# Performance work log

Measured on AMD Instinct MI355X. Metric: run time of the kernel, lower is better.

The kernel has to match this reference:

```python
import jax, jax.numpy as jnp
import numpy as np

B, T, D, HS = 8, 2048, 1024, 64  # batch, seq, num_embd, head_size


def setup_inputs() -> dict:
    key = jax.random.key(0)
    kc, kq, kk, kv = jax.random.split(key, 4)
    return {
        "context": jax.random.normal(kc, (B, T, D), dtype=jnp.float32),
        "Wq": jax.random.normal(kq, (D, HS), dtype=jnp.float32) * (D ** -0.5),
        "Wk": jax.random.normal(kk, (D, HS), dtype=jnp.float32) * (D ** -0.5),
        "Wv": jax.random.normal(kv, (D, HS), dtype=jnp.float32) * (D ** -0.5),
    }


def reference(context, Wq, Wk, Wv):
    # context: [B, T, D]; projections: [B, T, HS]
    q = context @ Wq
    k = context @ Wk
    v = context @ Wv
    scale = k.shape[-1] ** -0.5
    # scores: [B, T, T], causal mask, stable softmax (dropout p=0 -> identity)
    wei = jnp.einsum("btd,bsd->bts", q, k) * scale
    t = wei.shape[-1]
    causal = jnp.tril(jnp.ones((t, t), dtype=bool))
    wei = jnp.where(causal, wei, -jnp.inf)
    wei = jax.nn.softmax(wei, axis=-1)
    return jnp.einsum("bts,bsh->bth", wei, v)
```

## Files before the change

### kernel.cpp

```cpp
#include <hip/hip_runtime.h>
#include <math.h>

#define BB 8
#define TT 2048
#define DD 1024
#define HSZ 64

typedef __bf16 bf16_t;
typedef bf16_t bf16x8 __attribute__((ext_vector_type(8)));
typedef bf16_t bf16x4 __attribute__((ext_vector_type(4)));
typedef float f32x4 __attribute__((ext_vector_type(4)));

#define MFMA16(A, B, C) __builtin_amdgcn_mfma_f32_16x16x32_bf16(A, B, C, 0, 0, 0)


__global__ __launch_bounds__(256) void wt_convert(
    const float* __restrict__ Wq, const float* __restrict__ Wk,
    const float* __restrict__ Wv, bf16_t* __restrict__ Wtf)
{
    int id = blockIdx.x * 256 + threadIdx.x;
    int j = id & 7;
    int lane = (id >> 3) & 63;
    int chunk = (id >> 9) & 31;
    int nt = id >> 14;
    int l16 = lane & 15, quad = lane >> 4;
    int k = chunk * 32 + quad * 8 + j;
    int col = nt * 16 + l16;
    int m = col >> 6, ncol = col & 63;
    const float* W = (m == 0) ? Wq : (m == 1) ? Wk : Wv;
    float scl = (m == 0) ? 0.18033688f : 1.0f;
    Wtf[id] = (bf16_t)(W[k * HSZ + ncol] * scl);
}

__global__ __launch_bounds__(256, 2) void qkv_proj(
    const float* __restrict__ ctx, const bf16_t* __restrict__ Wtf,
    bf16_t* __restrict__ Q, bf16_t* __restrict__ Kf, bf16_t* __restrict__ Vf)
{
    __shared__ f32x4 red[4][12][64];

    const int tid = threadIdx.x;
    const int w = tid >> 6, lane = tid & 63;
    const int quad = lane >> 4, l16 = lane & 15;
    const size_t row0 = (size_t)blockIdx.x * 16;
    const int k0 = w * 256;

    f32x4 acc[12];
    #pragma unroll
    for (int i = 0; i < 12; ++i) acc[i] = (f32x4){0.f, 0.f, 0.f, 0.f};

    const float* arow = ctx + (row0 + l16) * DD + k0 + quad * 8;
    const bf16_t* wbase = Wtf + lane * 8;

    bf16x8 bfr[2][12];
    {
        const int chunk0 = k0 >> 5;
        #pragma unroll
        for (int nt = 0; nt < 12; ++nt)
            bfr[0][nt] = *(const bf16x8*)(wbase + ((size_t)nt * 32 + chunk0) * 512);
    }
    float4 a0 = *(const float4*)(arow);
    float4 a1 = *(const float4*)(arow + 4);

    #pragma unroll
    for (int kc = 0; kc < 256; kc += 32) {
        const int cur = (kc >> 5) & 1;
        bf16x8 af;
        af[0] = (bf16_t)a0.x; af[1] = (bf16_t)a0.y;
        af[2] = (bf16_t)a0.z; af[3] = (bf16_t)a0.w;
        af[4] = (bf16_t)a1.x; af[5] = (bf16_t)a1.y;
        af[6] = (bf16_t)a1.z; af[7] = (bf16_t)a1.w;

        if (kc + 32 < 256) {
            const int chunk = (k0 + kc + 32) >> 5;
            #pragma unroll
            for (int nt = 0; nt < 12; ++nt)
                bfr[cur ^ 1][nt] =
                    *(const bf16x8*)(wbase + ((size_t)nt * 32 + chunk) * 512);
            a0 = *(const float4*)(arow + kc + 32);
            a1 = *(const float4*)(arow + kc + 36);
        }

        #pragma unroll
        for (int nt = 0; nt < 12; ++nt)
            acc[nt] = MFMA16(af, bfr[cur][nt], acc[nt]);
    }

    #pragma unroll
    for (int nt = 0; nt < 12; ++nt) red[w][nt][lane] = acc[nt];
    __syncthreads();

    const int bb   = (int)(row0 >> 11);
    const int tloc = (int)(row0 & 2047);
    const int kt   = tloc >> 6;
    const int nn   = (tloc >> 4) & 3;

    #pragma unroll
    for (int i = 0; i < 3; ++i) {
        const int nt = w * 3 + i;
        f32x4 s = red[0][nt][lane];
        s += red[1][nt][lane];
        s += red[2][nt][lane];
        s += red[3][nt][lane];

        const int m = nt >> 2;
        if (m == 0) {
            const int col = (nt & 3) * 16 + l16;
            #pragma unroll
            for (int reg = 0; reg < 4; ++reg)
                Q[(row0 + quad * 4 + reg) * HSZ + col] = (bf16_t)s[reg];
        } else if (m == 1) {
            const int g = nt - 4;
            const int ks = g >> 1;
            const int quadf = (g & 1) * 2 + (l16 >> 3);
            const int jj = l16 & 7;
            const size_t fb = ((((size_t)bb * 32 + kt) * 4 + nn) * 2 + ks) * 512;
            #pragma unroll
            for (int reg = 0; reg < 4; ++reg)
                Kf[fb + (quadf * 16 + quad * 4 + reg) * 8 + jj] = (bf16_t)s[reg];
        } else {
            const int dt = nt - 8;
            const int t0 = tloc + quad * 4;
            const int ks = (t0 >> 5) & 1;
            const int quadf = (t0 >> 3) & 3;
            const int j0 = t0 & 7;
            const size_t fb = ((((size_t)bb * 32 + kt) * 2 + ks) * 4 + dt) * 512;
            bf16x4 v;
            #pragma unroll
            for (int reg = 0; reg < 4; ++reg) v[reg] = (bf16_t)s[reg];
            *(bf16x4*)(Vf + fb + (quadf * 16 + l16) * 8 + j0) = v;
        }
    }
}

__device__ __forceinline__ void load_kfrags(
    const bf16_t* __restrict__ Kf, size_t bofs, int kt, int lane, int nv,
    bf16x8* kf)
{
    const bf16_t* kbase = Kf + ((bofs + (size_t)kt) * 8) * 512 + lane * 8;
    #pragma unroll
    for (int n = 0; n < 4; ++n) {
        if (n < nv) {
            kf[2 * n]     = *(const bf16x8*)(kbase + (n * 2) * 512);
            kf[2 * n + 1] = *(const bf16x8*)(kbase + (n * 2 + 1) * 512);
        }
    }
}

__global__ __launch_bounds__(64, 3) void attn_kernel(
    const bf16_t* __restrict__ Q, const bf16_t* __restrict__ Kf,
    const bf16_t* __restrict__ Vf,
    float* __restrict__ Opart, float* __restrict__ Lpart)
{
    __shared__ bf16_t Ps[16][76];

    const int lane = threadIdx.x;
    const int quad = lane >> 4, l16 = lane & 15;

    const int z = blockIdx.x;
    const int b = z & 7, c = z >> 3;
    const int j = 127 - (c >> 2);
    const int seg = c & 3;
    const size_t base = (size_t)b * TT * HSZ;
    const size_t bofs = (size_t)b * 32;
    const int ntile = (j >> 2) + 1, jm = j & 3;

    const bf16_t* qp = Q + base + (size_t)(j * 16 + l16) * HSZ + quad * 8;
    bf16x8 qf0 = *(const bf16x8*)qp;
    bf16x8 qf1 = *(const bf16x8*)(qp + 32);

    bf16x8 onesf;
    {
        bf16_t e = (l16 == 0) ? (bf16_t)1.0f : (bf16_t)0.0f;
        #pragma unroll
        for (int i = 0; i < 8; ++i) onesf[i] = e;
    }

    f32x4 o[4];
    #pragma unroll
    for (int dt = 0; dt < 4; ++dt) o[dt] = (f32x4){0.f, 0.f, 0.f, 0.f};
    f32x4 lacc = (f32x4){0.f, 0.f, 0.f, 0.f};

    bf16x8 kA[8], kB[8];

    auto process = [&](int kt, const bf16x8* kf) {
        const bool last = (kt == ntile - 1);
        const int nv = last ? jm + 1 : 4;
        const int ksm = (nv > 2) ? 2 : 1;

        const bf16_t* vbase = Vf + ((bofs + (size_t)kt) * 8) * 512 + lane * 8;
        bf16x8 vf[8];
        #pragma unroll
        for (int dt = 0; dt < 4; ++dt) {
            vf[2 * dt] = *(const bf16x8*)(vbase + dt * 512);
            if (ksm == 2) vf[2 * dt + 1] = *(const bf16x8*)(vbase + (4 + dt) * 512);
        }

        f32x4 sc[4];
        #pragma unroll
        for (int n = 0; n < 4; ++n) {
            if (n < nv) {
                f32x4 a = (f32x4){0.f, 0.f, 0.f, 0.f};
                a = MFMA16(qf0, kf[2 * n], a);
                a = MFMA16(qf1, kf[2 * n + 1], a);
                sc[n] = a;
            }
        }

        if (last) {
            #pragma unroll
            for (int n = 0; n < 4; ++n) {
                if (n < nv) {
                    #pragma unroll
                    for (int reg = 0; reg < 4; ++reg) {
                        bool masked = (n == jm) && (l16 > quad * 4 + reg);
                        float p = __builtin_amdgcn_exp2f(sc[n][reg]);
                        sc[n][reg] = masked ? 0.f : p;
                    }
                }
            }
        } else {
            #pragma unroll
            for (int n = 0; n < 4; ++n)
                #pragma unroll
                for (int reg = 0; reg < 4; ++reg)
                    sc[n][reg] = __builtin_amdgcn_exp2f(sc[n][reg]);
        }

        #pragma unroll
        for (int n = 0; n < 4; ++n) {
            #pragma unroll
            for (int reg = 0; reg < 4; ++reg) {
                float p = (n < nv) ? sc[n][reg] : 0.f;
                Ps[quad * 4 + reg][n * 16 + l16] = (bf16_t)p;
            }
        }
        bf16x8 pf0 = *(const bf16x8*)&Ps[l16][quad * 8];
        bf16x8 pf1 = *(const bf16x8*)&Ps[l16][32 + quad * 8];

        #pragma unroll
        for (int dt = 0; dt < 4; ++dt) {
            o[dt] = MFMA16(pf0, vf[2 * dt], o[dt]);
            if (ksm == 2) o[dt] = MFMA16(pf1, vf[2 * dt + 1], o[dt]);
        }
        lacc = MFMA16(pf0, onesf, lacc);
        if (ksm == 2) lacc = MFMA16(pf1, onesf, lacc);
    };

    auto nv_of = [&](int kt) { return (kt == ntile - 1) ? jm + 1 : 4; };

    if (seg < ntile) {
        load_kfrags(Kf, bofs, seg, lane, nv_of(seg), kA);
        for (int kt = seg; kt < ntile; kt += 8) {
            if (kt + 4 < ntile) load_kfrags(Kf, bofs, kt + 4, lane, nv_of(kt + 4), kB);
            process(kt, kA);
            if (kt + 4 < ntile) {
                if (kt + 8 < ntile) load_kfrags(Kf, bofs, kt + 8, lane, nv_of(kt + 8), kA);
                process(kt + 4, kB);
            }
        }
    }

    float* op = Opart + (size_t)z * 16 * 64;
    #pragma unroll
    for (int dt = 0; dt < 4; ++dt) {
        #pragma unroll
        for (int reg = 0; reg < 4; ++reg)
            op[(quad * 4 + reg) * 64 + dt * 16 + l16] = o[dt][reg];
    }
    if (l16 == 0) {
        #pragma unroll
        for (int reg = 0; reg < 4; ++reg)
            Lpart[z * 16 + quad * 4 + reg] = lacc[reg];
    }
}

__global__ __launch_bounds__(256) void combine_kernel(
    const float* __restrict__ Opart, const float* __restrict__ Lpart,
    float* __restrict__ O)
{
    int gid = blockIdx.x * 256 + threadIdx.x;
    int col = gid & 63;
    int row = (gid >> 6) & 15;
    int j   = (gid >> 10) & 127;
    int b   = gid >> 17;
    int z0 = ((127 - j) * 4) * 8 + b;
    float l = 0.f, ov = 0.f;
    #pragma unroll
    for (int s = 0; s < 4; ++s) {
        l  += Lpart[(z0 + 8 * s) * 16 + row];
        ov += Opart[((size_t)(z0 + 8 * s) * 16 + row) * 64 + col];
    }
    O[((size_t)b * TT + j * 16 + row) * 64 + col] = ov / l;
}

extern "C" void kernel_launch(void* const* d_in, const int* in_sizes, int n_in,
                              void* d_out, int out_size, void* d_ws, size_t ws_size,
                              hipStream_t stream) {
    const float* ctx = (const float*)d_in[0];
    const float* Wq  = (const float*)d_in[1];
    const float* Wk  = (const float*)d_in[2];
    const float* Wv  = (const float*)d_in[3];
    float* out = (float*)d_out;

    const size_t NQ = (size_t)BB * TT * HSZ;
    bf16_t* Qw  = (bf16_t*)d_ws;
    bf16_t* Kfw = Qw + NQ;
    bf16_t* Vfw = Kfw + NQ;
    bf16_t* Wtf = Vfw + NQ;
    float*  Opart = (float*)(Wtf + 196608);
    float*  Lpart = Opart + (size_t)4096 * 1024;

    wt_convert<<<768, 256, 0, stream>>>(Wq, Wk, Wv, Wtf);
    qkv_proj<<<1024, 256, 0, stream>>>(ctx, Wtf, Qw, Kfw, Vfw);
    attn_kernel<<<4096, 64, 0, stream>>>(Qw, Kfw, Vfw, Opart, Lpart);
    combine_kernel<<<4096, 256, 0, stream>>>(Opart, Lpart, out);
}
```

Before: 140.4 us.

## Cut projection register/LDS footprint and make attention K/V loads unconditional

The QKV projection drops its double-buffered weight fragments and does its cross-wave reduction in three rounds through a smaller shared buffer. This allows three blocks per CU instead of two, at the cost of software prefetch and extra barriers. The attention kernel now always loads all eight K and V fragments, removing per-fragment branches. This may load data that is never used on the last causal tile, in exchange for simpler, more uniform load code.

```diff
diff --git a/kernel.cpp b/kernel.cpp
--- a/kernel.cpp
+++ b/kernel.cpp
@@ -32,11 +32,11 @@
     Wtf[id] = (bf16_t)(W[k * HSZ + ncol] * scl);
 }
 
-__global__ __launch_bounds__(256, 2) void qkv_proj(
+__global__ __launch_bounds__(256, 3) void qkv_proj(
     const float* __restrict__ ctx, const bf16_t* __restrict__ Wtf,
     bf16_t* __restrict__ Q, bf16_t* __restrict__ Kf, bf16_t* __restrict__ Vf)
 {
-    __shared__ f32x4 red[4][12][64];
+    __shared__ f32x4 red[4][4][64];
 
     const int tid = threadIdx.x;
     const int w = tid >> 6, lane = tid & 63;
@@ -51,43 +51,24 @@
     const float* arow = ctx + (row0 + l16) * DD + k0 + quad * 8;
     const bf16_t* wbase = Wtf + lane * 8;
 
-    bf16x8 bfr[2][12];
-    {
-        const int chunk0 = k0 >> 5;
+    #pragma unroll
+    for (int kc = 0; kc < 256; kc += 32) {
+        const int chunk = (k0 + kc) >> 5;
+        bf16x8 bfr[12];
         #pragma unroll
         for (int nt = 0; nt < 12; ++nt)
-            bfr[0][nt] = *(const bf16x8*)(wbase + ((size_t)nt * 32 + chunk0) * 512);
-    }
-    float4 a0 = *(const float4*)(arow);
-    float4 a1 = *(const float4*)(arow + 4);
-
-    #pragma unroll
-    for (int kc = 0; kc < 256; kc += 32) {
-        const int cur = (kc >> 5) & 1;
+            bfr[nt] = *(const bf16x8*)(wbase + ((size_t)nt * 32 + chunk) * 512);
+        float4 a0 = *(const float4*)(arow + kc);
+        float4 a1 = *(const float4*)(arow + kc + 4);
         bf16x8 af;
         af[0] = (bf16_t)a0.x; af[1] = (bf16_t)a0.y;
         af[2] = (bf16_t)a0.z; af[3] = (bf16_t)a0.w;
         af[4] = (bf16_t)a1.x; af[5] = (bf16_t)a1.y;
         af[6] = (bf16_t)a1.z; af[7] = (bf16_t)a1.w;
-
-        if (kc + 32 < 256) {
-            const int chunk = (k0 + kc + 32) >> 5;
-            #pragma unroll
-            for (int nt = 0; nt < 12; ++nt)
-                bfr[cur ^ 1][nt] =
-                    *(const bf16x8*)(wbase + ((size_t)nt * 32 + chunk) * 512);
-            a0 = *(const float4*)(arow + kc + 32);
-            a1 = *(const float4*)(arow + kc + 36);
-        }
-
         #pragma unroll
         for (int nt = 0; nt < 12; ++nt)
-            acc[nt] = MFMA16(af, bfr[cur][nt], acc[nt]);
-    }
-
-    #pragma unroll
-    for (int nt = 0; nt < 12; ++nt) red[w][nt][lane] = acc[nt];
-    __syncthreads();
+            acc[nt] = MFMA16(af, bfr[nt], acc[nt]);
+    }
 
     const int bb   = (int)(row0 >> 11);
     const int tloc = (int)(row0 & 2047);
@@ -95,35 +76,36 @@
     const int nn   = (tloc >> 4) & 3;
 
     #pragma unroll
-    for (int i = 0; i < 3; ++i) {
-        const int nt = w * 3 + i;
-        f32x4 s = red[0][nt][lane];
-        s += red[1][nt][lane];
-        s += red[2][nt][lane];
-        s += red[3][nt][lane];
-
-        const int m = nt >> 2;
-        if (m == 0) {
-            const int col = (nt & 3) * 16 + l16;
+    for (int r = 0; r < 3; ++r) {
+        if (r) __syncthreads();
+        #pragma unroll
+        for (int i = 0; i < 4; ++i) red[w][i][lane] = acc[r * 4 + i];
+        __syncthreads();
+
+        f32x4 s = red[0][w][lane];
+        s += red[1][w][lane];
+        s += red[2][w][lane];
+        s += red[3][w][lane];
+
+        if (r == 0) {
+            const int col = w * 16 + l16;
             #pragma unroll
             for (int reg = 0; reg < 4; ++reg)
                 Q[(row0 + quad * 4 + reg) * HSZ + col] = (bf16_t)s[reg];
-        } else if (m == 1) {
-            const int g = nt - 4;
-            const int ks = g >> 1;
-            const int quadf = (g & 1) * 2 + (l16 >> 3);
+        } else if (r == 1) {
+            const int ks = w >> 1;
+            const int quadf = (w & 1) * 2 + (l16 >> 3);
             const int jj = l16 & 7;
             const size_t fb = ((((size_t)bb * 32 + kt) * 4 + nn) * 2 + ks) * 512;
             #pragma unroll
             for (int reg = 0; reg < 4; ++reg)
                 Kf[fb + (quadf * 16 + quad * 4 + reg) * 8 + jj] = (bf16_t)s[reg];
         } else {
-            const int dt = nt - 8;
             const int t0 = tloc + quad * 4;
             const int ks = (t0 >> 5) & 1;
             const int quadf = (t0 >> 3) & 3;
             const int j0 = t0 & 7;
-            const size_t fb = ((((size_t)bb * 32 + kt) * 2 + ks) * 4 + dt) * 512;
+            const size_t fb = ((((size_t)bb * 32 + kt) * 2 + ks) * 4 + w) * 512;
             bf16x4 v;
             #pragma unroll
             for (int reg = 0; reg < 4; ++reg) v[reg] = (bf16_t)s[reg];
@@ -133,17 +115,12 @@
 }
 
 __device__ __forceinline__ void load_kfrags(
-    const bf16_t* __restrict__ Kf, size_t bofs, int kt, int lane, int nv,
-    bf16x8* kf)
+    const bf16_t* __restrict__ Kf, size_t bofs, int kt, int lane, bf16x8* kf)
 {
     const bf16_t* kbase = Kf + ((bofs + (size_t)kt) * 8) * 512 + lane * 8;
     #pragma unroll
-    for (int n = 0; n < 4; ++n) {
-        if (n < nv) {
-            kf[2 * n]     = *(const bf16x8*)(kbase + (n * 2) * 512);
-            kf[2 * n + 1] = *(const bf16x8*)(kbase + (n * 2 + 1) * 512);
-        }
-    }
+    for (int i = 0; i < 8; ++i)
+        kf[i] = *(const bf16x8*)(kbase + i * 512);
 }
 
 __global__ __launch_bounds__(64, 3) void attn_kernel(
@@ -190,10 +167,8 @@
         const bf16_t* vbase = Vf + ((bofs + (size_t)kt) * 8) * 512 + lane * 8;
         bf16x8 vf[8];
         #pragma unroll
-        for (int dt = 0; dt < 4; ++dt) {
-            vf[2 * dt] = *(const bf16x8*)(vbase + dt * 512);
-            if (ksm == 2) vf[2 * dt + 1] = *(const bf16x8*)(vbase + (4 + dt) * 512);
-        }
+        for (int i = 0; i < 8; ++i)
+            vf[i] = *(const bf16x8*)(vbase + i * 512);
 
         f32x4 sc[4];
         #pragma unroll
@@ -239,22 +214,20 @@
 
         #pragma unroll
         for (int dt = 0; dt < 4; ++dt) {
-            o[dt] = MFMA16(pf0, vf[2 * dt], o[dt]);
-            if (ksm == 2) o[dt] = MFMA16(pf1, vf[2 * dt + 1], o[dt]);
+            o[dt] = MFMA16(pf0, vf[dt], o[dt]);
+            if (ksm == 2) o[dt] = MFMA16(pf1, vf[4 + dt], o[dt]);
         }
         lacc = MFMA16(pf0, onesf, lacc);
         if (ksm == 2) lacc = MFMA16(pf1, onesf, lacc);
     };
 
-    auto nv_of = [&](int kt) { return (kt == ntile - 1) ? jm + 1 : 4; };
-
     if (seg < ntile) {
-        load_kfrags(Kf, bofs, seg, lane, nv_of(seg), kA);
+        load_kfrags(Kf, bofs, seg, lane, kA);
         for (int kt = seg; kt < ntile; kt += 8) {
-            if (kt + 4 < ntile) load_kfrags(Kf, bofs, kt + 4, lane, nv_of(kt + 4), kB);
+            if (kt + 4 < ntile) load_kfrags(Kf, bofs, kt + 4, lane, kB);
             process(kt, kA);
             if (kt + 4 < ntile) {
-                if (kt + 8 < ntile) load_kfrags(Kf, bofs, kt + 8, lane, nv_of(kt + 8), kA);
+                if (kt + 8 < ntile) load_kfrags(Kf, bofs, kt + 8, lane, kA);
                 process(kt + 4, kB);
             }
         }
```

Result: slower. 143.7 us (+2.4%).
